# Kernel optimization log

Measured on AMD Instinct MI355X. Metric: run time of the kernel, lower is better.

## Reference

```python
import jax, jax.numpy as jnp
import numpy as np

DIM = 1024
DEPTH = 6
HEADS = 16
MLP = 4096
HEAD_DIM = DIM // HEADS
SCALE = HEAD_DIM ** -0.5
EPS = 1e-5


def _ln(x, g, b):
    m = jnp.mean(x, axis=-1, keepdims=True)
    v = jnp.mean(jnp.square(x - m), axis=-1, keepdims=True)
    return (x - m) * jax.lax.rsqrt(v + EPS) * g + b


def setup_inputs() -> dict:
    key = jax.random.key(0)
    ks = jax.random.split(key, 16)
    B, N = 4, 1024
    s_d = 1.0 / np.sqrt(DIM)
    s_m = 1.0 / np.sqrt(MLP)
    inp = {
        "x1": jax.random.normal(ks[0], (B, N, DIM), jnp.float32),
        "x2": jax.random.normal(ks[1], (B, N, DIM), jnp.float32),
        # stacked per-layer params; Linear weights stored as [in, out]
        "ln1_g": jnp.ones((DEPTH, DIM), jnp.float32),
        "ln1_b": jnp.zeros((DEPTH, DIM), jnp.float32),
        "wq": jax.random.normal(ks[2], (DEPTH, DIM, DIM), jnp.float32) * s_d,
        "wk": jax.random.normal(ks[3], (DEPTH, DIM, DIM), jnp.float32) * s_d,
        "wv": jax.random.normal(ks[4], (DEPTH, DIM, DIM), jnp.float32) * s_d,
        "wo": jax.random.normal(ks[5], (DEPTH, DIM, DIM), jnp.float32) * s_d,
        "bo": jnp.zeros((DEPTH, DIM), jnp.float32),
        "ln2_g": jnp.ones((DEPTH, DIM), jnp.float32),
        "ln2_b": jnp.zeros((DEPTH, DIM), jnp.float32),
        "w1": jax.random.normal(ks[6], (DEPTH, DIM, MLP), jnp.float32) * s_d,
        "b1": jnp.zeros((DEPTH, MLP), jnp.float32),
        "w2": jax.random.normal(ks[7], (DEPTH, MLP, DIM), jnp.float32) * s_m,
        "b2": jnp.zeros((DEPTH, DIM), jnp.float32),
    }
    return inp


def _split_heads(t):
    b, n, _ = t.shape
    return t.reshape(b, n, HEADS, HEAD_DIM).transpose(0, 2, 1, 3)  # b h n d


def reference(x1, x2, ln1_g, ln1_b, wq, wk, wv, wo, bo, ln2_g, ln2_b, w1, b1, w2, b2):
    # dropout disabled (eval mode)
    for i in range(DEPTH):
        # PreNorm(MCA): same LayerNorm params applied to x1 and x2
        n1 = _ln(x1, ln1_g[i], ln1_b[i])
        n2 = _ln(x2, ln1_g[i], ln1_b[i])
        q = _split_heads(n1 @ wq[i])
        k = _split_heads(n2 @ wk[i])
        v = _split_heads(n2 @ wv[i])
        dots = jnp.einsum('bhqd,bhkd->bhqk', q, k) * SCALE
        attn = jax.nn.softmax(dots, axis=-1)
        out = jnp.einsum('bhqk,bhkd->bhqd', attn, v)
        b, h, n, d = out.shape
        out = out.transpose(0, 2, 1, 3).reshape(b, n, h * d)
        x1 = out @ wo[i] + bo[i] + x1
        # PreNorm(FeedForward)
        nf = _ln(x1, ln2_g[i], ln2_b[i])
        hdn = jax.nn.gelu(nf @ w1[i] + b1[i], approximate=False)
        x1 = hdn @ w2[i] + b2[i] + x1
    return x1
```

## Files before the change

kernel.cpp:

```cpp
#include <hip/hip_runtime.h>
#include <stdint.h>

#define N_SEQ 1024
#define N_TOK 4096
#define ATT_SCALE 0.125f

typedef unsigned short u16;
typedef __attribute__((ext_vector_type(8))) short short8;
typedef __attribute__((ext_vector_type(4))) short short4v;
typedef __attribute__((ext_vector_type(4))) float f32x4;

__device__ __forceinline__ u16 f2bf(float f) {
  uint32_t u = __float_as_uint(f);
  u += 0x7fffu + ((u >> 16) & 1u);
  return (u16)(u >> 16);
}

__device__ __forceinline__ void gload16(const void* g, void* lds) {
  __builtin_amdgcn_global_load_lds(
      (const __attribute__((address_space(1))) unsigned int*)g,
      (__attribute__((address_space(3))) unsigned int*)lds, 16, 0, 0);
}

__global__ void copy_f32_kernel(const float* __restrict__ in, float* __restrict__ out) {
  int i = blockIdx.x * 256 + threadIdx.x;
  ((float4*)out)[i] = ((const float4*)in)[i];
}

__global__ __launch_bounds__(256) void tconv_kernel(const float* __restrict__ src,
                                                    u16* __restrict__ dst,
                                                    int K, int NN, size_t dstLS) {
  __shared__ u16 tile[64][68];
  int n0 = blockIdx.x * 64, k0 = blockIdx.y * 64, L = blockIdx.z;
  const float* s = src + (size_t)L * K * NN;
  u16* d = dst + (size_t)L * dstLS;
  int t = threadIdx.x;
  int rr = t >> 4, cc = (t & 15) * 4;
#pragma unroll
  for (int ii = 0; ii < 4; ii++) {
    int kl = rr + ii * 16;
    float4 v = *(const float4*)&s[(size_t)(k0 + kl) * NN + n0 + cc];
    tile[cc + 0][kl] = f2bf(v.x);
    tile[cc + 1][kl] = f2bf(v.y);
    tile[cc + 2][kl] = f2bf(v.z);
    tile[cc + 3][kl] = f2bf(v.w);
  }
  __syncthreads();
#pragma unroll
  for (int ii = 0; ii < 4; ii++) {
    int nl = rr + ii * 16;
    short4v o;
    o.x = (short)tile[nl][cc + 0];
    o.y = (short)tile[nl][cc + 1];
    o.z = (short)tile[nl][cc + 2];
    o.w = (short)tile[nl][cc + 3];
    *(short4v*)&d[(size_t)(n0 + nl) * K + k0 + cc] = o;
  }
}

__global__ __launch_bounds__(256) void ln_kernel(const float* __restrict__ x,
                                                 const float* __restrict__ g,
                                                 const float* __restrict__ b,
                                                 u16* __restrict__ out) {
  int row = blockIdx.x;
  const float* xr = x + (size_t)row * 1024;
  int t = threadIdx.x;
  float4 v = *(const float4*)&xr[t * 4];
  float s = v.x + v.y + v.z + v.w;
  float sq = v.x * v.x + v.y * v.y + v.z * v.z + v.w * v.w;
#pragma unroll
  for (int m = 1; m < 64; m <<= 1) {
    s += __shfl_xor(s, m, 64);
    sq += __shfl_xor(sq, m, 64);
  }
  __shared__ float ps[8];
  int w = t >> 6;
  if ((t & 63) == 0) { ps[w] = s; ps[4 + w] = sq; }
  __syncthreads();
  s = ps[0] + ps[1] + ps[2] + ps[3];
  sq = ps[4] + ps[5] + ps[6] + ps[7];
  float mean = s * (1.0f / 1024.0f);
  float var = sq * (1.0f / 1024.0f) - mean * mean;
  float rs = rsqrtf(var + 1e-5f);
  float4 gv = *(const float4*)&g[t * 4];
  float4 bv = *(const float4*)&b[t * 4];
  short4v o;
  o.x = (short)f2bf((v.x - mean) * rs * gv.x + bv.x);
  o.y = (short)f2bf((v.y - mean) * rs * gv.y + bv.y);
  o.z = (short)f2bf((v.z - mean) * rs * gv.z + bv.z);
  o.w = (short)f2bf((v.w - mean) * rs * gv.w + bv.w);
  *(short4v*)&out[(size_t)row * 1024 + t * 4] = o;
}

template <int BM, int BN, int WM, int WN, int MAXB, int MODE>
__global__ __launch_bounds__(WM * WN * 64, MAXB) void gemmS(const u16* __restrict__ A,
                                                            const u16* __restrict__ Bt,
                                                            u16* __restrict__ outb,
                                                            float* __restrict__ outf,
                                                            const float* __restrict__ bias,
                                                            const float* __restrict__ resid,
                                                            int N, int K,
                                                            size_t zA, size_t zB, size_t zC) {
  constexpr int BK = 64;
  constexpr int NW = WM * WN;
  constexpr int T = NW * 64;
  constexpr int WTM = BM / WM, WTN = BN / WN;
  constexpr int FM = WTM / 16, FN = WTN / 16;
  constexpr int AT = BM * BK, BTL = BN * BK;
  constexpr int LA = AT / 8 / T, LB = BTL / 8 / T;
  __shared__ u16 smem[2 * (AT + BTL)];

  int t = threadIdx.x, lane = t & 63, w = t >> 6;
  int wm = w / WN, wn = w % WN;
  size_t z = blockIdx.z;
  const u16* Ag = A + z * zA + (size_t)(blockIdx.y * BM) * K;
  const u16* Bg = Bt + z * zB + (size_t)(blockIdx.x * BN) * K;
  f32x4 acc[FM][FN] = {};

  auto stage = [&](int d, int k0) {
    u16* ab = smem + d * (AT + BTL);
    u16* bb = ab + AT;
#pragma unroll
    for (int l = 0; l < LA; l++) {
      int c = (l * NW + w) * 64 + lane;
      int r = c >> 3, s = c & 7;
      gload16(Ag + (size_t)r * K + k0 + ((s ^ (r & 7)) << 3), ab + (l * NW + w) * 512);
    }
#pragma unroll
    for (int l = 0; l < LB; l++) {
      int c = (l * NW + w) * 64 + lane;
      int r = c >> 3, s = c & 7;
      gload16(Bg + (size_t)r * K + k0 + ((s ^ (r & 7)) << 3), bb + (l * NW + w) * 512);
    }
  };

  auto rdA = [&](const u16* ab, int mi, int ks) {
    int rr = wm * WTM + mi * 16 + (lane & 15);
    int j = ks * 4 + (lane >> 4);
    return *(const short8*)&ab[rr * BK + ((j ^ (rr & 7)) << 3)];
  };
  auto rdB = [&](const u16* bb, int ni, int ks) {
    int rr = wn * WTN + ni * 16 + (lane & 15);
    int j = ks * 4 + (lane >> 4);
    return *(const short8*)&bb[rr * BK + ((j ^ (rr & 7)) << 3)];
  };

  const int NT = K / BK;
  stage(0, 0);
  __syncthreads();

  int buf = 0;
  for (int tt = 0; tt < NT; tt++) {
    if (tt + 1 < NT) stage(buf ^ 1, (tt + 1) * BK);
    const u16* ab = smem + buf * (AT + BTL);
    const u16* bb = ab + AT;
    short8 af[2][FM], bfr[2][FN];
#pragma unroll
    for (int ks = 0; ks < 2; ks++) {
#pragma unroll
      for (int mi = 0; mi < FM; mi++) af[ks][mi] = rdA(ab, mi, ks);
#pragma unroll
      for (int ni = 0; ni < FN; ni++) bfr[ks][ni] = rdB(bb, ni, ks);
    }
#pragma unroll
    for (int ks = 0; ks < 2; ks++)
#pragma unroll
      for (int mi = 0; mi < FM; mi++)
#pragma unroll
        for (int ni = 0; ni < FN; ni++)
          acc[mi][ni] = __builtin_amdgcn_mfma_f32_16x16x32_bf16(af[ks][mi], bfr[ks][ni],
                                                                acc[mi][ni], 0, 0, 0);
    __syncthreads();
    buf ^= 1;
  }

  int r0 = blockIdx.y * BM + wm * WTM + ((lane >> 4) << 2);
  int c0 = blockIdx.x * BN + wn * WTN + (lane & 15);
#pragma unroll
  for (int mi = 0; mi < FM; mi++) {
#pragma unroll
    for (int r = 0; r < 4; r++) {
      size_t row = (size_t)(r0 + mi * 16 + r);
#pragma unroll
      for (int ni = 0; ni < FN; ni++) {
        size_t col = (size_t)(c0 + ni * 16);
        size_t idx = z * zC + row * N + col;
        float val = acc[mi][ni][r];
        if (MODE == 0) {
          outb[idx] = f2bf(val);
        } else if (MODE == 1) {
          outf[idx] = val + bias[col] + resid[idx];
        } else {
          float xg = val + bias[col];
          outb[idx] = f2bf(0.5f * xg * (1.0f + erff(xg * 0.70710678f)));
        }
      }
    }
  }
}

template <int BM, int BN, int WM, int WN, int MODE>
__global__ __launch_bounds__(WM * WN * 64, 2) void gemm8(const u16* __restrict__ A,
                                                         const u16* __restrict__ Bt,
                                                         u16* __restrict__ outb,
                                                         float* __restrict__ outf,
                                                         const float* __restrict__ bias,
                                                         const float* __restrict__ resid,
                                                         int N, int K) {
  constexpr int BK = 64;
  constexpr int NW = WM * WN;
  constexpr int T = NW * 64;
  constexpr int WTM = BM / WM, WTN = BN / WN;
  constexpr int FM = WTM / 16, FN = WTN / 16, HM = FM / 2;
  constexpr int AT = BM * BK, BTL = BN * BK;
  constexpr int LA = AT / 8 / T, LB = BTL / 8 / T;
  constexpr int LTOT = LA + LB;
  __shared__ u16 smem[2 * (AT + BTL)];

  int t = threadIdx.x, lane = t & 63, w = t >> 6;
  int wm = w / WN, wn = w % WN;
  const u16* Ag = A + (size_t)(blockIdx.y * BM) * K;
  const u16* Bg = Bt + (size_t)(blockIdx.x * BN) * K;
  f32x4 acc[FM][FN] = {};

  auto stage = [&](int d, int k0) {
    u16* ab = smem + d * (AT + BTL);
    u16* bb = ab + AT;
#pragma unroll
    for (int l = 0; l < LA; l++) {
      int c = (l * NW + w) * 64 + lane;
      int r = c >> 3, s = c & 7;
      gload16(Ag + (size_t)r * K + k0 + ((s ^ (r & 7)) << 3), ab + (l * NW + w) * 512);
    }
#pragma unroll
    for (int l = 0; l < LB; l++) {
      int c = (l * NW + w) * 64 + lane;
      int r = c >> 3, s = c & 7;
      gload16(Bg + (size_t)r * K + k0 + ((s ^ (r & 7)) << 3), bb + (l * NW + w) * 512);
    }
  };

  auto rdA = [&](const u16* ab, int mi, int ks) {
    int rr = wm * WTM + mi * 16 + (lane & 15);
    int j = ks * 4 + (lane >> 4);
    return *(const short8*)&ab[rr * BK + ((j ^ (rr & 7)) << 3)];
  };
  auto rdB = [&](const u16* bb, int ni, int ks) {
    int rr = wn * WTN + ni * 16 + (lane & 15);
    int j = ks * 4 + (lane >> 4);
    return *(const short8*)&bb[rr * BK + ((j ^ (rr & 7)) << 3)];
  };

  const int NT = K / BK;
  stage(0, 0);
  stage(1, BK);
  __builtin_amdgcn_sched_barrier(0);

  int buf = 0;
  for (int tt = 0; tt < NT; tt++) {
    asm volatile("s_waitcnt vmcnt(%0)" ::"n"(LTOT) : "memory");
    __builtin_amdgcn_s_barrier();
    __builtin_amdgcn_sched_barrier(0);
    const u16* ab = smem + buf * (AT + BTL);
    const u16* bb = ab + AT;
    short8 b0[FN], a0lo[HM], a0hi[HM], b1[FN], a1lo[HM], a1hi[HM];
#pragma unroll
    for (int n = 0; n < FN; n++) b0[n] = rdB(bb, n, 0);
#pragma unroll
    for (int m = 0; m < HM; m++) a0lo[m] = rdA(ab, m, 0);
#pragma unroll
    for (int m = 0; m < HM; m++) a0hi[m] = rdA(ab, HM + m, 0);
    asm volatile("s_waitcnt lgkmcnt(%0)" ::"n"(HM) : "memory");
    __builtin_amdgcn_sched_barrier(0);
#pragma unroll
    for (int n = 0; n < FN; n++) b1[n] = rdB(bb, n, 1);
#pragma unroll
    for (int m = 0; m < HM; m++) a1lo[m] = rdA(ab, m, 1);
    __builtin_amdgcn_s_setprio(1);
#pragma unroll
    for (int m = 0; m < HM; m++)
#pragma unroll
      for (int n = 0; n < FN; n++)
        acc[m][n] = __builtin_amdgcn_mfma_f32_16x16x32_bf16(a0lo[m], b0[n], acc[m][n], 0, 0, 0);
    __builtin_amdgcn_s_setprio(0);
    asm volatile("s_waitcnt lgkmcnt(%0)" ::"n"(FN + HM) : "memory");
    __builtin_amdgcn_sched_barrier(0);
#pragma unroll
    for (int m = 0; m < HM; m++) a1hi[m] = rdA(ab, HM + m, 1);
    __builtin_amdgcn_s_setprio(1);
#pragma unroll
    for (int m = 0; m < HM; m++)
#pragma unroll
      for (int n = 0; n < FN; n++)
        acc[HM + m][n] = __builtin_amdgcn_mfma_f32_16x16x32_bf16(a0hi[m], b0[n], acc[HM + m][n], 0, 0, 0);
    __builtin_amdgcn_s_setprio(0);
    asm volatile("s_waitcnt lgkmcnt(%0)" ::"n"(HM) : "memory");
    __builtin_amdgcn_sched_barrier(0);
    __builtin_amdgcn_s_setprio(1);
#pragma unroll
    for (int m = 0; m < HM; m++)
#pragma unroll
      for (int n = 0; n < FN; n++)
        acc[m][n] = __builtin_amdgcn_mfma_f32_16x16x32_bf16(a1lo[m], b1[n], acc[m][n], 0, 0, 0);
    __builtin_amdgcn_s_setprio(0);
    asm volatile("s_waitcnt lgkmcnt(0)" ::: "memory");
    __builtin_amdgcn_sched_barrier(0);
    __builtin_amdgcn_s_barrier();
    __builtin_amdgcn_sched_barrier(0);
    stage(buf, ((tt + 2) % NT) * BK);
    __builtin_amdgcn_sched_barrier(0);
    __builtin_amdgcn_s_setprio(1);
#pragma unroll
    for (int m = 0; m < HM; m++)
#pragma unroll
      for (int n = 0; n < FN; n++)
        acc[HM + m][n] = __builtin_amdgcn_mfma_f32_16x16x32_bf16(a1hi[m], b1[n], acc[HM + m][n], 0, 0, 0);
    __builtin_amdgcn_s_setprio(0);
    buf ^= 1;
  }

  int r0 = blockIdx.y * BM + wm * WTM + ((lane >> 4) << 2);
  int c0 = blockIdx.x * BN + wn * WTN + (lane & 15);
#pragma unroll
  for (int mi = 0; mi < FM; mi++) {
#pragma unroll
    for (int r = 0; r < 4; r++) {
      size_t row = (size_t)(r0 + mi * 16 + r);
#pragma unroll
      for (int ni = 0; ni < FN; ni++) {
        size_t col = (size_t)(c0 + ni * 16);
        size_t idx = row * N + col;
        float val = acc[mi][ni][r];
        if (MODE == 0) {
          outb[idx] = f2bf(val);
        } else if (MODE == 1) {
          outf[idx] = val + bias[col] + resid[idx];
        } else {
          float xg = val + bias[col];
          outb[idx] = f2bf(0.5f * xg * (1.0f + erff(xg * 0.70710678f)));
        }
      }
    }
  }
}

__global__ __launch_bounds__(256, 4) void attn_kernel(const u16* __restrict__ qb,
                                                      const u16* __restrict__ kvb,
                                                      u16* __restrict__ ob) {
  int qt = blockIdx.x, bh = blockIdx.y;
  int b = bh >> 4, h = bh & 15;
  int t = threadIdx.x, lane = t & 63, w = t >> 6;
  __shared__ u16 Qs[64 * 64];
  __shared__ u16 Ks[64 * 64];
  __shared__ u16 Vt[64 * 64];
  __shared__ u16 Ps[4][16 * 64];

  const u16* qbase = qb + (size_t)b * N_SEQ * 1024 + h * 64;
  const u16* kbase = kvb + (size_t)b * N_SEQ * 2048 + h * 64;
  const u16* vbase = kbase + 1024;
  u16* obase = ob + (size_t)b * N_SEQ * 1024 + h * 64;

  int r = t >> 2, c = (t & 3) * 16;
  {
    const u16* src = qbase + (size_t)(qt * 64 + r) * 1024 + c;
    *(short8*)&Qs[r * 64 + c] = *(const short8*)src;
    *(short8*)&Qs[r * 64 + c + 8] = *(const short8*)(src + 8);
  }
  short8 kreg0, kreg1, vreg0, vreg1;
  {
    const u16* ksrc = kbase + (size_t)r * 2048 + c;
    kreg0 = *(const short8*)ksrc;
    kreg1 = *(const short8*)(ksrc + 8);
    const u16* vsrc = vbase + (size_t)r * 2048 + c;
    vreg0 = *(const short8*)vsrc;
    vreg1 = *(const short8*)(vsrc + 8);
  }
  __syncthreads();
  short8 qa0 = *(const short8*)&Qs[(w * 16 + (lane & 15)) * 64 + (lane >> 4) * 8];
  short8 qa1 = *(const short8*)&Qs[(w * 16 + (lane & 15)) * 64 + 32 + (lane >> 4) * 8];

  f32x4 o[4] = {};
  float m_r[4] = {-1e30f, -1e30f, -1e30f, -1e30f};
  float l_r[4] = {0.0f, 0.0f, 0.0f, 0.0f};

  for (int kt = 0; kt < 16; kt++) {
    if (kt > 0) __syncthreads();
    {
      int jj0 = c >> 3;
      *(short8*)&Ks[r * 64 + ((jj0 ^ (r & 7)) << 3)] = kreg0;
      *(short8*)&Ks[r * 64 + (((jj0 + 1) ^ (r & 7)) << 3)] = kreg1;
#pragma unroll
      for (int j = 0; j < 8; j++) {
        int row = c + j, rowb = c + 8 + j;
        Vt[row * 64 + (((r >> 3) ^ (row & 7)) << 3) + (r & 7)] = (u16)vreg0[j];
        Vt[rowb * 64 + (((r >> 3) ^ (rowb & 7)) << 3) + (r & 7)] = (u16)vreg1[j];
      }
    }
    __syncthreads();
    if (kt < 15) {
      const u16* ksrc = kbase + (size_t)((kt + 1) * 64 + r) * 2048 + c;
      kreg0 = *(const short8*)ksrc;
      kreg1 = *(const short8*)(ksrc + 8);
      const u16* vsrc = vbase + (size_t)((kt + 1) * 64 + r) * 2048 + c;
      vreg0 = *(const short8*)vsrc;
      vreg1 = *(const short8*)(vsrc + 8);
    }

    f32x4 s[4] = {};
#pragma unroll
    for (int kb = 0; kb < 4; kb++) {
      int key = kb * 16 + (lane & 15);
      int jj = lane >> 4;
      short8 k0 = *(const short8*)&Ks[key * 64 + ((jj ^ (key & 7)) << 3)];
      short8 k1 = *(const short8*)&Ks[key * 64 + (((4 + jj) ^ (key & 7)) << 3)];
      s[kb] = __builtin_amdgcn_mfma_f32_16x16x32_bf16(qa0, k0, s[kb], 0, 0, 0);
      s[kb] = __builtin_amdgcn_mfma_f32_16x16x32_bf16(qa1, k1, s[kb], 0, 0, 0);
    }
    float fac[4], rowsum[4];
#pragma unroll
    for (int rr = 0; rr < 4; rr++) {
      float a = fmaxf(fmaxf(s[0][rr], s[1][rr]), fmaxf(s[2][rr], s[3][rr])) * ATT_SCALE;
      a = fmaxf(a, __shfl_xor(a, 1, 64));
      a = fmaxf(a, __shfl_xor(a, 2, 64));
      a = fmaxf(a, __shfl_xor(a, 4, 64));
      a = fmaxf(a, __shfl_xor(a, 8, 64));
      float mn = fmaxf(m_r[rr], a);
      fac[rr] = __expf(m_r[rr] - mn);
      m_r[rr] = mn;
      rowsum[rr] = 0.0f;
    }
#pragma unroll
    for (int kb = 0; kb < 4; kb++) {
      int chunk = 2 * kb + ((lane & 15) >> 3);
#pragma unroll
      for (int rr = 0; rr < 4; rr++) {
        float p = __expf(s[kb][rr] * ATT_SCALE - m_r[rr]);
        rowsum[rr] += p;
        int row = (lane >> 4) * 4 + rr;
        Ps[w][row * 64 + ((chunk ^ (row & 7)) << 3) + (lane & 7)] = f2bf(p);
      }
    }
#pragma unroll
    for (int rr = 0; rr < 4; rr++) {
      float rs = rowsum[rr];
      rs += __shfl_xor(rs, 1, 64);
      rs += __shfl_xor(rs, 2, 64);
      rs += __shfl_xor(rs, 4, 64);
      rs += __shfl_xor(rs, 8, 64);
      l_r[rr] = l_r[rr] * fac[rr] + rs;
      o[0][rr] *= fac[rr];
      o[1][rr] *= fac[rr];
      o[2][rr] *= fac[rr];
      o[3][rr] *= fac[rr];
    }
#pragma unroll
    for (int ks = 0; ks < 2; ks++) {
      int rowp = lane & 15;
      int jj = 4 * ks + (lane >> 4);
      short8 pf = *(const short8*)&Ps[w][rowp * 64 + ((jj ^ (rowp & 7)) << 3)];
#pragma unroll
      for (int db = 0; db < 4; db++) {
        int row = db * 16 + (lane & 15);
        short8 vf = *(const short8*)&Vt[row * 64 + ((jj ^ (row & 7)) << 3)];
        o[db] = __builtin_amdgcn_mfma_f32_16x16x32_bf16(pf, vf, o[db], 0, 0, 0);
      }
    }
  }
#pragma unroll
  for (int rr = 0; rr < 4; rr++) {
    float inv = 1.0f / l_r[rr];
    size_t row = (size_t)(qt * 64 + w * 16 + (lane >> 4) * 4 + rr);
#pragma unroll
    for (int db = 0; db < 4; db++)
      obase[row * 1024 + db * 16 + (lane & 15)] = f2bf(o[db][rr] * inv);
  }
}

extern "C" void kernel_launch(void* const* d_in, const int* in_sizes, int n_in,
                              void* d_out, int out_size, void* d_ws, size_t ws_size,
                              hipStream_t stream) {
  const float* x1 = (const float*)d_in[0];
  const float* x2 = (const float*)d_in[1];
  const float* ln1_g = (const float*)d_in[2];
  const float* ln1_b = (const float*)d_in[3];
  const float* wq = (const float*)d_in[4];
  const float* wk = (const float*)d_in[5];
  const float* wv = (const float*)d_in[6];
  const float* wo = (const float*)d_in[7];
  const float* bo = (const float*)d_in[8];
  const float* ln2_g = (const float*)d_in[9];
  const float* ln2_b = (const float*)d_in[10];
  const float* w1 = (const float*)d_in[11];
  const float* b1 = (const float*)d_in[12];
  const float* w2 = (const float*)d_in[13];
  const float* b2 = (const float*)d_in[14];
  float* xout = (float*)d_out;

  u16* p = (u16*)d_ws;
  u16* wqt = p;   p += (size_t)6 * 1024 * 1024;
  u16* kvt = p;   p += (size_t)6 * 2048 * 1024;
  u16* wot = p;   p += (size_t)6 * 1024 * 1024;
  u16* w1t = p;   p += (size_t)6 * 4096 * 1024;
  u16* w2t = p;   p += (size_t)6 * 1024 * 4096;
  u16* n1 = p;    p += (size_t)N_TOK * 1024;
  u16* n2all = p; p += (size_t)6 * N_TOK * 1024;
  u16* qbuf = p;  p += (size_t)N_TOK * 1024;
  u16* kvb6 = p;  p += (size_t)6 * N_TOK * 2048;
  u16* ao = p;    p += (size_t)N_TOK * 1024;
  u16* hid = p;   p += (size_t)N_TOK * 4096;

  dim3 blk(256);
  tconv_kernel<<<dim3(16, 16, 6), blk, 0, stream>>>(wq, wqt, 1024, 1024, (size_t)1024 * 1024);
  tconv_kernel<<<dim3(16, 16, 6), blk, 0, stream>>>(wk, kvt, 1024, 1024, (size_t)2048 * 1024);
  tconv_kernel<<<dim3(16, 16, 6), blk, 0, stream>>>(wv, kvt + (size_t)1024 * 1024, 1024, 1024, (size_t)2048 * 1024);
  tconv_kernel<<<dim3(16, 16, 6), blk, 0, stream>>>(wo, wot, 1024, 1024, (size_t)1024 * 1024);
  tconv_kernel<<<dim3(64, 16, 6), blk, 0, stream>>>(w1, w1t, 1024, 4096, (size_t)4096 * 1024);
  tconv_kernel<<<dim3(16, 64, 6), blk, 0, stream>>>(w2, w2t, 4096, 1024, (size_t)1024 * 4096);
  copy_f32_kernel<<<4096, blk, 0, stream>>>(x1, xout);

  for (int i = 0; i < 6; i++)
    ln_kernel<<<N_TOK, blk, 0, stream>>>(x2, ln1_g + i * 1024, ln1_b + i * 1024,
                                         n2all + (size_t)i * N_TOK * 1024);
  gemmS<64, 128, 2, 2, 3, 0><<<dim3(16, 64, 6), blk, 0, stream>>>(
      n2all, kvt, kvb6, nullptr, nullptr, nullptr, 2048, 1024,
      (size_t)N_TOK * 1024, (size_t)2048 * 1024, (size_t)N_TOK * 2048);

  for (int i = 0; i < 6; i++) {
    ln_kernel<<<N_TOK, blk, 0, stream>>>(xout, ln1_g + i * 1024, ln1_b + i * 1024, n1);
    gemm8<128, 64, 2, 2, 0><<<dim3(16, 32), blk, 0, stream>>>(
        n1, wqt + (size_t)i * 1024 * 1024, qbuf, nullptr, nullptr, nullptr, 1024, 1024);
    attn_kernel<<<dim3(16, 64), blk, 0, stream>>>(qbuf, kvb6 + (size_t)i * N_TOK * 2048, ao);
    gemm8<128, 64, 2, 2, 1><<<dim3(16, 32), blk, 0, stream>>>(
        ao, wot + (size_t)i * 1024 * 1024, nullptr, xout, bo + i * 1024, xout, 1024, 1024);
    ln_kernel<<<N_TOK, blk, 0, stream>>>(xout, ln2_g + i * 1024, ln2_b + i * 1024, n1);
    gemmS<64, 128, 2, 2, 3, 2><<<dim3(32, 64), blk, 0, stream>>>(
        n1, w1t + (size_t)i * 4096 * 1024, hid, nullptr, b1 + i * 4096, nullptr, 4096, 1024, 0, 0, 0);
    gemm8<128, 64, 2, 2, 1><<<dim3(16, 32), blk, 0, stream>>>(
        hid, w2t + (size_t)i * 1024 * 4096, nullptr, xout, b2 + i * 1024, xout, 1024, 4096);
  }
}
```

Baseline: 1.585 ms.

## Replace gemmS with 256x256 eight-wave GEMM using interleaved LDS reads and MFMA

Replaces the generic gemmS kernel, used for the KV projection and the FFN up-projection with GELU, with a 256x256 tile, 512-thread kernel. Each wave computes a 128x64 sub-tile. The main loop keeps two stages in flight with explicit vmcnt/lgkmcnt waits, sched barriers and setprio around MFMA groups, interleaving LDS fragment reads with matrix math. The larger tiles give more data reuse per global load, but produce far fewer blocks (256 for the FFN GEMM), which risks poor CU fill on a 256-CU part, plus heavy register pressure. The tail loop also issues wrapped-around stage loads that are never used.

```diff
diff --git a/kernel.cpp b/kernel.cpp
--- a/kernel.cpp
+++ b/kernel.cpp
@@ -92,97 +92,131 @@
   *(short4v*)&out[(size_t)row * 1024 + t * 4] = o;
 }
 
-template <int BM, int BN, int WM, int WN, int MAXB, int MODE>
-__global__ __launch_bounds__(WM * WN * 64, MAXB) void gemmS(const u16* __restrict__ A,
-                                                            const u16* __restrict__ Bt,
-                                                            u16* __restrict__ outb,
-                                                            float* __restrict__ outf,
-                                                            const float* __restrict__ bias,
-                                                            const float* __restrict__ resid,
-                                                            int N, int K,
-                                                            size_t zA, size_t zB, size_t zC) {
+template <int MODE>
+__global__ __launch_bounds__(512, 2) void gemm256(const u16* __restrict__ A,
+                                                  const u16* __restrict__ Bt,
+                                                  u16* __restrict__ outb,
+                                                  float* __restrict__ outf,
+                                                  const float* __restrict__ bias,
+                                                  const float* __restrict__ resid,
+                                                  int N, int K,
+                                                  size_t zA, size_t zB, size_t zC) {
   constexpr int BK = 64;
-  constexpr int NW = WM * WN;
-  constexpr int T = NW * 64;
-  constexpr int WTM = BM / WM, WTN = BN / WN;
-  constexpr int FM = WTM / 16, FN = WTN / 16;
-  constexpr int AT = BM * BK, BTL = BN * BK;
-  constexpr int LA = AT / 8 / T, LB = BTL / 8 / T;
-  __shared__ u16 smem[2 * (AT + BTL)];
+  constexpr int AT = 256 * BK;
+  __shared__ u16 smem[2 * 2 * AT];
 
   int t = threadIdx.x, lane = t & 63, w = t >> 6;
-  int wm = w / WN, wn = w % WN;
+  int wm = w >> 2, wn = w & 3;
   size_t z = blockIdx.z;
-  const u16* Ag = A + z * zA + (size_t)(blockIdx.y * BM) * K;
-  const u16* Bg = Bt + z * zB + (size_t)(blockIdx.x * BN) * K;
-  f32x4 acc[FM][FN] = {};
+  const u16* Ag = A + z * zA + (size_t)(blockIdx.y * 256) * K;
+  const u16* Bg = Bt + z * zB + (size_t)(blockIdx.x * 256) * K;
+  f32x4 acc[8][4] = {};
 
   auto stage = [&](int d, int k0) {
-    u16* ab = smem + d * (AT + BTL);
+    u16* ab = smem + d * 2 * AT;
     u16* bb = ab + AT;
 #pragma unroll
-    for (int l = 0; l < LA; l++) {
-      int c = (l * NW + w) * 64 + lane;
+    for (int l = 0; l < 4; l++) {
+      int c = (l * 8 + w) * 64 + lane;
       int r = c >> 3, s = c & 7;
-      gload16(Ag + (size_t)r * K + k0 + ((s ^ (r & 7)) << 3), ab + (l * NW + w) * 512);
-    }
-#pragma unroll
-    for (int l = 0; l < LB; l++) {
-      int c = (l * NW + w) * 64 + lane;
+      gload16(Ag + (size_t)r * K + k0 + ((s ^ (r & 7)) << 3), ab + (l * 8 + w) * 512);
+    }
+#pragma unroll
+    for (int l = 0; l < 4; l++) {
+      int c = (l * 8 + w) * 64 + lane;
       int r = c >> 3, s = c & 7;
-      gload16(Bg + (size_t)r * K + k0 + ((s ^ (r & 7)) << 3), bb + (l * NW + w) * 512);
+      gload16(Bg + (size_t)r * K + k0 + ((s ^ (r & 7)) << 3), bb + (l * 8 + w) * 512);
     }
   };
 
   auto rdA = [&](const u16* ab, int mi, int ks) {
-    int rr = wm * WTM + mi * 16 + (lane & 15);
+    int rr = wm * 128 + mi * 16 + (lane & 15);
     int j = ks * 4 + (lane >> 4);
     return *(const short8*)&ab[rr * BK + ((j ^ (rr & 7)) << 3)];
   };
   auto rdB = [&](const u16* bb, int ni, int ks) {
-    int rr = wn * WTN + ni * 16 + (lane & 15);
+    int rr = wn * 64 + ni * 16 + (lane & 15);
     int j = ks * 4 + (lane >> 4);
     return *(const short8*)&bb[rr * BK + ((j ^ (rr & 7)) << 3)];
   };
 
   const int NT = K / BK;
   stage(0, 0);
-  __syncthreads();
-
-  int buf = 0;
+  stage(1, BK);
+  __builtin_amdgcn_sched_barrier(0);
+
   for (int tt = 0; tt < NT; tt++) {
-    if (tt + 1 < NT) stage(buf ^ 1, (tt + 1) * BK);
-    const u16* ab = smem + buf * (AT + BTL);
+    int sl = tt & 1;
+    asm volatile("s_waitcnt vmcnt(8)" ::: "memory");
+    __builtin_amdgcn_s_barrier();
+    __builtin_amdgcn_sched_barrier(0);
+    const u16* ab = smem + sl * 2 * AT;
     const u16* bb = ab + AT;
-    short8 af[2][FM], bfr[2][FN];
-#pragma unroll
-    for (int ks = 0; ks < 2; ks++) {
-#pragma unroll
-      for (int mi = 0; mi < FM; mi++) af[ks][mi] = rdA(ab, mi, ks);
-#pragma unroll
-      for (int ni = 0; ni < FN; ni++) bfr[ks][ni] = rdB(bb, ni, ks);
-    }
-#pragma unroll
-    for (int ks = 0; ks < 2; ks++)
-#pragma unroll
-      for (int mi = 0; mi < FM; mi++)
-#pragma unroll
-        for (int ni = 0; ni < FN; ni++)
-          acc[mi][ni] = __builtin_amdgcn_mfma_f32_16x16x32_bf16(af[ks][mi], bfr[ks][ni],
-                                                                acc[mi][ni], 0, 0, 0);
-    __syncthreads();
-    buf ^= 1;
-  }
-
-  int r0 = blockIdx.y * BM + wm * WTM + ((lane >> 4) << 2);
-  int c0 = blockIdx.x * BN + wn * WTN + (lane & 15);
-#pragma unroll
-  for (int mi = 0; mi < FM; mi++) {
+    short8 b0[4], a0lo[4], a0hi[4], b1[4], a1lo[4], a1hi[4];
+#pragma unroll
+    for (int n = 0; n < 4; n++) b0[n] = rdB(bb, n, 0);
+#pragma unroll
+    for (int m = 0; m < 4; m++) a0lo[m] = rdA(ab, m, 0);
+#pragma unroll
+    for (int m = 0; m < 4; m++) a0hi[m] = rdA(ab, 4 + m, 0);
+#pragma unroll
+    for (int n = 0; n < 4; n++) b1[n] = rdB(bb, n, 1);
+#pragma unroll
+    for (int m = 0; m < 4; m++) a1lo[m] = rdA(ab, m, 1);
+    asm volatile("s_waitcnt lgkmcnt(12)" ::: "memory");
+    __builtin_amdgcn_sched_barrier(0);
+    __builtin_amdgcn_s_setprio(1);
+#pragma unroll
+    for (int m = 0; m < 4; m++)
+#pragma unroll
+      for (int n = 0; n < 4; n++)
+        acc[m][n] = __builtin_amdgcn_mfma_f32_16x16x32_bf16(a0lo[m], b0[n], acc[m][n], 0, 0, 0);
+    __builtin_amdgcn_s_setprio(0);
+    asm volatile("s_waitcnt lgkmcnt(8)" ::: "memory");
+    __builtin_amdgcn_sched_barrier(0);
+    __builtin_amdgcn_s_setprio(1);
+#pragma unroll
+    for (int m = 0; m < 4; m++)
+#pragma unroll
+      for (int n = 0; n < 4; n++)
+        acc[4 + m][n] = __builtin_amdgcn_mfma_f32_16x16x32_bf16(a0hi[m], b0[n], acc[4 + m][n], 0, 0, 0);
+    __builtin_amdgcn_s_setprio(0);
+#pragma unroll
+    for (int m = 0; m < 4; m++) a1hi[m] = rdA(ab, 4 + m, 1);
+    asm volatile("s_waitcnt lgkmcnt(4)" ::: "memory");
+    __builtin_amdgcn_sched_barrier(0);
+    __builtin_amdgcn_s_setprio(1);
+#pragma unroll
+    for (int m = 0; m < 4; m++)
+#pragma unroll
+      for (int n = 0; n < 4; n++)
+        acc[m][n] = __builtin_amdgcn_mfma_f32_16x16x32_bf16(a1lo[m], b1[n], acc[m][n], 0, 0, 0);
+    __builtin_amdgcn_s_setprio(0);
+    asm volatile("s_waitcnt lgkmcnt(0)" ::: "memory");
+    __builtin_amdgcn_sched_barrier(0);
+    __builtin_amdgcn_s_barrier();
+    __builtin_amdgcn_sched_barrier(0);
+    stage(sl, ((tt + 2) % NT) * BK);
+    __builtin_amdgcn_sched_barrier(0);
+    __builtin_amdgcn_s_setprio(1);
+#pragma unroll
+    for (int m = 0; m < 4; m++)
+#pragma unroll
+      for (int n = 0; n < 4; n++)
+        acc[4 + m][n] = __builtin_amdgcn_mfma_f32_16x16x32_bf16(a1hi[m], b1[n], acc[4 + m][n], 0, 0, 0);
+    __builtin_amdgcn_s_setprio(0);
+  }
+  asm volatile("s_waitcnt vmcnt(0)" ::: "memory");
+
+  int r0 = blockIdx.y * 256 + wm * 128 + ((lane >> 4) << 2);
+  int c0 = blockIdx.x * 256 + wn * 64 + (lane & 15);
+#pragma unroll
+  for (int mi = 0; mi < 8; mi++) {
 #pragma unroll
     for (int r = 0; r < 4; r++) {
       size_t row = (size_t)(r0 + mi * 16 + r);
 #pragma unroll
-      for (int ni = 0; ni < FN; ni++) {
+      for (int ni = 0; ni < 4; ni++) {
         size_t col = (size_t)(c0 + ni * 16);
         size_t idx = z * zC + row * N + col;
         float val = acc[mi][ni][r];
@@ -521,7 +555,7 @@
   for (int i = 0; i < 6; i++)
     ln_kernel<<<N_TOK, blk, 0, stream>>>(x2, ln1_g + i * 1024, ln1_b + i * 1024,
                                          n2all + (size_t)i * N_TOK * 1024);
-  gemmS<64, 128, 2, 2, 3, 0><<<dim3(16, 64, 6), blk, 0, stream>>>(
+  gemm256<0><<<dim3(8, 16, 6), dim3(512), 0, stream>>>(
       n2all, kvt, kvb6, nullptr, nullptr, nullptr, 2048, 1024,
       (size_t)N_TOK * 1024, (size_t)2048 * 1024, (size_t)N_TOK * 2048);
 
@@ -533,7 +567,7 @@
     gemm8<128, 64, 2, 2, 1><<<dim3(16, 32), blk, 0, stream>>>(
         ao, wot + (size_t)i * 1024 * 1024, nullptr, xout, bo + i * 1024, xout, 1024, 1024);
     ln_kernel<<<N_TOK, blk, 0, stream>>>(xout, ln2_g + i * 1024, ln2_b + i * 1024, n1);
-    gemmS<64, 128, 2, 2, 3, 2><<<dim3(32, 64), blk, 0, stream>>>(
+    gemm256<2><<<dim3(16, 16), dim3(512), 0, stream>>>(
         n1, w1t + (size_t)i * 4096 * 1024, hid, nullptr, b1 + i * 4096, nullptr, 4096, 1024, 0, 0, 0);
     gemm8<128, 64, 2, 2, 1><<<dim3(16, 32), blk, 0, stream>>>(
         hid, w2t + (size_t)i * 1024 * 4096, nullptr, xout, b2 + i * 1024, xout, 1024, 4096);
```

Result: slower. 1.704 ms (+7.5%).
